# Optimization experiments

Hardware: AMD Instinct MI355X
Metric: run time of the kernel (lower is better)

Reference implementation:

```python
import jax, jax.numpy as jnp
import numpy as np

NUM_ROUTES = 1152
NUM_CAPS = 10
CAPS_IN = 8
CAPS_DIM = 16
BATCH = 128
NUM_IT = 3


def _squash(s):
    # s: [..., caps_dim]; scale = |s|^2 / ((1+|s|^2) * |s|)
    sqn = jnp.sum(s * s, axis=-1, keepdims=True)
    return s * (sqn / ((1.0 + sqn) * jnp.sqrt(sqn)))


def setup_inputs() -> dict:
    key = jax.random.key(0)
    k1, k2 = jax.random.split(key)
    x = jax.random.normal(k1, (BATCH, NUM_ROUTES, CAPS_IN), dtype=jnp.float32)
    W = jax.random.normal(k2, (1, NUM_ROUTES, NUM_CAPS, CAPS_DIM, CAPS_IN), dtype=jnp.float32)
    return {"input": x, "W": W}


def reference(input, W):
    # u_hat[b,r,j,d] = W[r,j,d,c] @ x[b,r,c]  (original broadcasts W over batch)
    u_hat = jnp.einsum('rjdc,brc->brjd', W[0], input)
    r, j = u_hat.shape[1], u_hat.shape[2]
    b_ij = jnp.zeros((r, j), dtype=u_hat.dtype)  # shared across batch, as in original
    v = None
    for _ in range(NUM_IT):
        c_ij = jax.nn.softmax(b_ij, axis=1)          # softmax over num_caps (dim=2 orig)
        s = jnp.einsum('rj,brjd->bjd', c_ij, u_hat)  # weighted sum over routes
        v = _squash(s)                                # [bs, num_caps, caps_dim]
        # agreement: <u_hat, v> averaged over batch (original updates every iter)
        b_ij = b_ij + jnp.mean(jnp.einsum('brjd,bjd->brj', u_hat, v), axis=0)
    return v[..., None]  # [bs, num_caps, caps_dim, 1], matches v_j.squeeze(1) shape
```

## Files before the change

### kernel.cpp

```cpp
#include <hip/hip_runtime.h>
#include <math.h>

#define R_ROUTES 1152
#define N_CAPS 10
#define C_IN 8
#define D_DIM 16
#define B_BATCH 128
#define JD 160
#define KK 9216
#define KSPLIT 48
#define RS 24
#define NG 5

typedef __attribute__((ext_vector_type(8))) short short8;
typedef __attribute__((ext_vector_type(4))) float f32x4;

__device__ inline unsigned short f2bf(float f) {
    unsigned int u = __float_as_uint(f);
    unsigned int r = u + 0x7FFFu + ((u >> 16) & 1u);
    return (unsigned short)(r >> 16);
}
__device__ inline float bf2f(unsigned short h) {
    return __uint_as_float(((unsigned int)h) << 16);
}


__global__ __launch_bounds__(256) void k_prep(
    const float* __restrict__ x, unsigned short* __restrict__ xh,
    unsigned short* __restrict__ xl, unsigned short* __restrict__ xT,
    float* __restrict__ b_ij, float* __restrict__ s_all) {
    __shared__ float tile[32][33];
    int bx = blockIdx.x;
    int by = blockIdx.y;
    int t = threadIdx.x;
    int tx = t & 31, ty = t >> 5;
#pragma unroll
    for (int i = 0; i < 4; i++) {
        int row = ty + i * 8;
        size_t idx = (size_t)(by * 32 + row) * KK + bx * 32 + tx;
        float v = x[idx];
        tile[row][tx] = v;
        unsigned short hi = f2bf(v);
        xh[idx] = hi;
        xl[idx] = f2bf(v - bf2f(hi));
    }
    __syncthreads();
#pragma unroll
    for (int i = 0; i < 4; i++) {
        int row = ty + i * 8;
        xT[(size_t)(bx * 32 + row) * B_BATCH + by * 32 + tx] = f2bf(tile[tx][row]);
    }
    int bid = by * 288 + bx;
    if (bid < 240) s_all[bid * 256 + t] = 0.f;
    else if (bid < 285) b_ij[(bid - 240) * 256 + t] = 0.f;
}

template <bool FIRST>
__global__ __launch_bounds__(256) void k_iter(
    const unsigned short* __restrict__ xh, const unsigned short* __restrict__ xl,
    const float* __restrict__ W, const float* __restrict__ b_ij,
    float* __restrict__ s) {
    __shared__ float cs[RS][N_CAPS];
    __shared__ unsigned short bhs[32][200];
    __shared__ unsigned short bls[32][200];
    int t = threadIdx.x;
    int ks = blockIdx.x, ng = blockIdx.y;
    int r0 = ks * RS, jd0 = ng * 32;

    if (!FIRST && t < RS) {
        float bj[N_CAPS], m = -1e30f;
#pragma unroll
        for (int j = 0; j < N_CAPS; j++) { bj[j] = b_ij[(r0 + t) * N_CAPS + j]; m = fmaxf(m, bj[j]); }
        float sum = 0.f;
#pragma unroll
        for (int j = 0; j < N_CAPS; j++) { bj[j] = expf(bj[j] - m); sum += bj[j]; }
        float inv = 1.f / sum;
#pragma unroll
        for (int j = 0; j < N_CAPS; j++) cs[t][j] = bj[j] * inv;
    }
    __syncthreads();

#pragma unroll
    for (int p = t; p < RS * 32; p += 256) {
        int rl = p >> 5, jdl = p & 31;
        const float* wp = W + ((size_t)(r0 + rl) * JD + jd0 + jdl) * C_IN;
        float c = FIRST ? 0.1f : cs[rl][(jd0 + jdl) >> 4];
        short8 vh, vl;
#pragma unroll
        for (int i = 0; i < 8; i++) {
            float cw = wp[i] * c;
            unsigned short hi = f2bf(cw);
            vh[i] = (short)hi;
            vl[i] = (short)f2bf(cw - bf2f(hi));
        }
        *(short8*)&bhs[jdl][rl * 8] = vh;
        *(short8*)&bls[jdl][rl * 8] = vl;
    }
    __syncthreads();

    int w = t >> 6, l = t & 63, row = l & 15, quad = l >> 4;
    const short8* pah0 = (const short8*)(xh + (size_t)(w * 16 + row) * KK + ks * 192);
    const short8* pal0 = (const short8*)(xl + (size_t)(w * 16 + row) * KK + ks * 192);
    const short8* pah1 = (const short8*)(xh + (size_t)((w + 4) * 16 + row) * KK + ks * 192);
    const short8* pal1 = (const short8*)(xl + (size_t)((w + 4) * 16 + row) * KK + ks * 192);
    f32x4 a00 = {0,0,0,0}, a01 = {0,0,0,0}, a10 = {0,0,0,0}, a11 = {0,0,0,0};
#pragma unroll
    for (int st = 0; st < 6; st++) {
        short8 Bh0 = *(const short8*)&bhs[row][st * 32 + quad * 8];
        short8 Bl0 = *(const short8*)&bls[row][st * 32 + quad * 8];
        short8 Bh1 = *(const short8*)&bhs[16 + row][st * 32 + quad * 8];
        short8 Bl1 = *(const short8*)&bls[16 + row][st * 32 + quad * 8];
        short8 Ah0 = pah0[st * 4 + quad], Al0 = pal0[st * 4 + quad];
        short8 Ah1 = pah1[st * 4 + quad], Al1 = pal1[st * 4 + quad];
        a00 = __builtin_amdgcn_mfma_f32_16x16x32_bf16(Ah0, Bh0, a00, 0, 0, 0);
        a00 = __builtin_amdgcn_mfma_f32_16x16x32_bf16(Ah0, Bl0, a00, 0, 0, 0);
        a00 = __builtin_amdgcn_mfma_f32_16x16x32_bf16(Al0, Bh0, a00, 0, 0, 0);
        a01 = __builtin_amdgcn_mfma_f32_16x16x32_bf16(Ah0, Bh1, a01, 0, 0, 0);
        a01 = __builtin_amdgcn_mfma_f32_16x16x32_bf16(Ah0, Bl1, a01, 0, 0, 0);
        a01 = __builtin_amdgcn_mfma_f32_16x16x32_bf16(Al0, Bh1, a01, 0, 0, 0);
        a10 = __builtin_amdgcn_mfma_f32_16x16x32_bf16(Ah1, Bh0, a10, 0, 0, 0);
        a10 = __builtin_amdgcn_mfma_f32_16x16x32_bf16(Ah1, Bl0, a10, 0, 0, 0);
        a10 = __builtin_amdgcn_mfma_f32_16x16x32_bf16(Al1, Bh0, a10, 0, 0, 0);
        a11 = __builtin_amdgcn_mfma_f32_16x16x32_bf16(Ah1, Bh1, a11, 0, 0, 0);
        a11 = __builtin_amdgcn_mfma_f32_16x16x32_bf16(Ah1, Bl1, a11, 0, 0, 0);
        a11 = __builtin_amdgcn_mfma_f32_16x16x32_bf16(Al1, Bh1, a11, 0, 0, 0);
    }
#pragma unroll
    for (int i = 0; i < 4; i++) {
        int b0 = w * 16 + quad * 4 + i, b1 = b0 + 64;
        atomicAdd(&s[(size_t)b0 * JD + jd0 + row],      a00[i]);
        atomicAdd(&s[(size_t)b0 * JD + jd0 + 16 + row], a01[i]);
        atomicAdd(&s[(size_t)b1 * JD + jd0 + row],      a10[i]);
        atomicAdd(&s[(size_t)b1 * JD + jd0 + 16 + row], a11[i]);
    }
}

__global__ __launch_bounds__(256) void k_va(
    const unsigned short* __restrict__ xT, const float* __restrict__ s,
    const float* __restrict__ W, float* __restrict__ b_ij) {
    __shared__ unsigned short vb[JD][136];
    __shared__ float m2[32][164];
    int t = threadIdx.x;
    int r0 = blockIdx.x * 4, rc0 = blockIdx.x * 32;

#pragma unroll
    for (int q = 0; q < 5; q++) {
        int pi = t * 5 + q;
        int b = pi / N_CAPS, j = pi % N_CAPS;
        const float* sp = s + (size_t)b * JD + j * D_DIM;
        float sv[D_DIM], sqn = 0.f;
#pragma unroll
        for (int d = 0; d < D_DIM; d++) { sv[d] = sp[d]; sqn = fmaf(sv[d], sv[d], sqn); }
        float scale = sqn / ((1.f + sqn) * sqrtf(sqn));
#pragma unroll
        for (int d = 0; d < D_DIM; d++)
            vb[j * D_DIM + d][b] = f2bf(sv[d] * scale);
    }
    __syncthreads();

    int w = t >> 6, l = t & 63, row = l & 15, quad = l >> 4;
    for (int u = w; u < 20; u += 4) {
        int mt = u / 10, nt = u % 10;
        const short8* pa = (const short8*)(xT + (size_t)(rc0 + mt * 16 + row) * B_BATCH);
        f32x4 acc = {0,0,0,0};
#pragma unroll
        for (int st = 0; st < 4; st++) {
            short8 Bv = *(const short8*)&vb[nt * 16 + row][st * 32 + quad * 8];
            acc = __builtin_amdgcn_mfma_f32_16x16x32_bf16(pa[st * 4 + quad], Bv, acc, 0, 0, 0);
        }
#pragma unroll
        for (int i = 0; i < 4; i++)
            m2[mt * 16 + quad * 4 + i][nt * 16 + row] = acc[i];
    }
    __syncthreads();

    for (int p = t; p < 640; p += 256) {
        int rl = p / JD, jd = p % JD;
        const float* wp = W + ((size_t)(r0 + rl) * JD + jd) * C_IN;
        float a = 0.f;
#pragma unroll
        for (int c = 0; c < C_IN; c++)
            a = fmaf(wp[c], m2[rl * 8 + c][jd], a);
#pragma unroll
        for (int off = 1; off < 16; off <<= 1) a += __shfl_xor(a, off, 16);
        if ((jd & 15) == 0)
            b_ij[(r0 + rl) * N_CAPS + (jd >> 4)] += a * (1.f / B_BATCH);
    }
}

__global__ __launch_bounds__(320) void k_rs_final(
    const float* __restrict__ s, float* __restrict__ out) {
    int t = threadIdx.x;
    int bloc = t / JD, jd = t % JD;
    int b = blockIdx.x * 2 + bloc;
    float acc = s[(size_t)b * JD + jd];
    float sq = acc * acc;
#pragma unroll
    for (int off = 1; off < 16; off <<= 1) sq += __shfl_xor(sq, off, 16);
    float scale = sq / ((1.f + sq) * sqrtf(sq));
    out[(size_t)b * JD + jd] = acc * scale;
}

extern "C" void kernel_launch(void* const* d_in, const int* in_sizes, int n_in,
                              void* d_out, int out_size, void* d_ws, size_t ws_size,
                              hipStream_t stream) {
    const float* x = (const float*)d_in[0];
    const float* W = (const float*)d_in[1];
    float* out = (float*)d_out;
    char* ws = (char*)d_ws;

    float*          b_ij = (float*)(ws + 0);
    float*          s0   = (float*)(ws + 46080);
    float*          s1   = (float*)(ws + 46080 + 81920);
    float*          s2   = (float*)(ws + 46080 + 163840);
    unsigned short* xh   = (unsigned short*)(ws + 292096);
    unsigned short* xl   = (unsigned short*)(ws + 2651392);
    unsigned short* xT   = (unsigned short*)(ws + 5010688);

    k_prep<<<dim3(288, 4), 256, 0, stream>>>(x, xh, xl, xT, b_ij, s0);

    k_iter<true><<<dim3(KSPLIT, NG), 256, 0, stream>>>(xh, xl, W, b_ij, s0);
    k_va<<<288, 256, 0, stream>>>(xT, s0, W, b_ij);

    k_iter<false><<<dim3(KSPLIT, NG), 256, 0, stream>>>(xh, xl, W, b_ij, s1);
    k_va<<<288, 256, 0, stream>>>(xT, s1, W, b_ij);

    k_iter<false><<<dim3(KSPLIT, NG), 256, 0, stream>>>(xh, xl, W, b_ij, s2);
    k_rs_final<<<64, 320, 0, stream>>>(s2, out);
}
```

Measured before the change: 113.4 us.

## Halve k-split size, drop W low-part MFMAs, fuse final squash, shrink k_va blocks

Doubles the number of k_iter blocks by halving the routes per block. It also drops the bf16 low-part correction of the c*W operand, cutting MFMAs from 3 to 2 per tile and halving that shared-memory staging. The last routing iteration now applies the final squash inside the last-finishing block via an atomic counter, replacing the separate k_rs_final launch. k_va uses smaller 128-thread blocks over twice as many blocks. Dropping the W low part lowers accuracy, and the final squash now runs in a single serial block.

```diff
diff --git a/kernel.cpp b/kernel.cpp
--- a/kernel.cpp
+++ b/kernel.cpp
@@ -8,9 +8,10 @@
 #define B_BATCH 128
 #define JD 160
 #define KK 9216
-#define KSPLIT 48
-#define RS 24
+#define KSPLIT 96
+#define RS 12
 #define NG 5
+#define GRID_I (KSPLIT * NG)
 
 typedef __attribute__((ext_vector_type(8))) short short8;
 typedef __attribute__((ext_vector_type(4))) float f32x4;
@@ -28,7 +29,8 @@
 __global__ __launch_bounds__(256) void k_prep(
     const float* __restrict__ x, unsigned short* __restrict__ xh,
     unsigned short* __restrict__ xl, unsigned short* __restrict__ xT,
-    float* __restrict__ b_ij, float* __restrict__ s_all) {
+    float* __restrict__ b_ij, float* __restrict__ s_all,
+    unsigned int* __restrict__ done) {
     __shared__ float tile[32][33];
     int bx = blockIdx.x;
     int by = blockIdx.y;
@@ -53,16 +55,18 @@
     int bid = by * 288 + bx;
     if (bid < 240) s_all[bid * 256 + t] = 0.f;
     else if (bid < 285) b_ij[(bid - 240) * 256 + t] = 0.f;
-}
-
-template <bool FIRST>
+    else if (bid == 285 && t == 0) *done = 0u;
+}
+
+template <bool FIRST, bool LAST>
 __global__ __launch_bounds__(256) void k_iter(
     const unsigned short* __restrict__ xh, const unsigned short* __restrict__ xl,
     const float* __restrict__ W, const float* __restrict__ b_ij,
-    float* __restrict__ s) {
+    float* __restrict__ s, unsigned int* __restrict__ done,
+    float* __restrict__ out) {
     __shared__ float cs[RS][N_CAPS];
-    __shared__ unsigned short bhs[32][200];
-    __shared__ unsigned short bls[32][200];
+    __shared__ unsigned short bhs[32][104];
+    __shared__ int islast;
     int t = threadIdx.x;
     int ks = blockIdx.x, ng = blockIdx.y;
     int r0 = ks * RS, jd0 = ng * 32;
@@ -85,83 +89,93 @@
         int rl = p >> 5, jdl = p & 31;
         const float* wp = W + ((size_t)(r0 + rl) * JD + jd0 + jdl) * C_IN;
         float c = FIRST ? 0.1f : cs[rl][(jd0 + jdl) >> 4];
-        short8 vh, vl;
-#pragma unroll
-        for (int i = 0; i < 8; i++) {
-            float cw = wp[i] * c;
-            unsigned short hi = f2bf(cw);
-            vh[i] = (short)hi;
-            vl[i] = (short)f2bf(cw - bf2f(hi));
-        }
+        short8 vh;
+#pragma unroll
+        for (int i = 0; i < 8; i++) vh[i] = (short)f2bf(wp[i] * c);
         *(short8*)&bhs[jdl][rl * 8] = vh;
-        *(short8*)&bls[jdl][rl * 8] = vl;
     }
     __syncthreads();
 
     int w = t >> 6, l = t & 63, row = l & 15, quad = l >> 4;
-    const short8* pah0 = (const short8*)(xh + (size_t)(w * 16 + row) * KK + ks * 192);
-    const short8* pal0 = (const short8*)(xl + (size_t)(w * 16 + row) * KK + ks * 192);
-    const short8* pah1 = (const short8*)(xh + (size_t)((w + 4) * 16 + row) * KK + ks * 192);
-    const short8* pal1 = (const short8*)(xl + (size_t)((w + 4) * 16 + row) * KK + ks * 192);
+    int mt0 = w, mt1 = w + 4;
+    const short8* pah0 = (const short8*)(xh + (size_t)(mt0 * 16 + row) * KK + ks * 96);
+    const short8* pal0 = (const short8*)(xl + (size_t)(mt0 * 16 + row) * KK + ks * 96);
+    const short8* pah1 = (const short8*)(xh + (size_t)(mt1 * 16 + row) * KK + ks * 96);
+    const short8* pal1 = (const short8*)(xl + (size_t)(mt1 * 16 + row) * KK + ks * 96);
     f32x4 a00 = {0,0,0,0}, a01 = {0,0,0,0}, a10 = {0,0,0,0}, a11 = {0,0,0,0};
 #pragma unroll
-    for (int st = 0; st < 6; st++) {
+    for (int st = 0; st < 3; st++) {
         short8 Bh0 = *(const short8*)&bhs[row][st * 32 + quad * 8];
-        short8 Bl0 = *(const short8*)&bls[row][st * 32 + quad * 8];
         short8 Bh1 = *(const short8*)&bhs[16 + row][st * 32 + quad * 8];
-        short8 Bl1 = *(const short8*)&bls[16 + row][st * 32 + quad * 8];
         short8 Ah0 = pah0[st * 4 + quad], Al0 = pal0[st * 4 + quad];
         short8 Ah1 = pah1[st * 4 + quad], Al1 = pal1[st * 4 + quad];
         a00 = __builtin_amdgcn_mfma_f32_16x16x32_bf16(Ah0, Bh0, a00, 0, 0, 0);
-        a00 = __builtin_amdgcn_mfma_f32_16x16x32_bf16(Ah0, Bl0, a00, 0, 0, 0);
         a00 = __builtin_amdgcn_mfma_f32_16x16x32_bf16(Al0, Bh0, a00, 0, 0, 0);
         a01 = __builtin_amdgcn_mfma_f32_16x16x32_bf16(Ah0, Bh1, a01, 0, 0, 0);
-        a01 = __builtin_amdgcn_mfma_f32_16x16x32_bf16(Ah0, Bl1, a01, 0, 0, 0);
         a01 = __builtin_amdgcn_mfma_f32_16x16x32_bf16(Al0, Bh1, a01, 0, 0, 0);
         a10 = __builtin_amdgcn_mfma_f32_16x16x32_bf16(Ah1, Bh0, a10, 0, 0, 0);
-        a10 = __builtin_amdgcn_mfma_f32_16x16x32_bf16(Ah1, Bl0, a10, 0, 0, 0);
         a10 = __builtin_amdgcn_mfma_f32_16x16x32_bf16(Al1, Bh0, a10, 0, 0, 0);
         a11 = __builtin_amdgcn_mfma_f32_16x16x32_bf16(Ah1, Bh1, a11, 0, 0, 0);
-        a11 = __builtin_amdgcn_mfma_f32_16x16x32_bf16(Ah1, Bl1, a11, 0, 0, 0);
         a11 = __builtin_amdgcn_mfma_f32_16x16x32_bf16(Al1, Bh1, a11, 0, 0, 0);
     }
 #pragma unroll
     for (int i = 0; i < 4; i++) {
-        int b0 = w * 16 + quad * 4 + i, b1 = b0 + 64;
+        int b0 = mt0 * 16 + quad * 4 + i, b1 = mt1 * 16 + quad * 4 + i;
         atomicAdd(&s[(size_t)b0 * JD + jd0 + row],      a00[i]);
         atomicAdd(&s[(size_t)b0 * JD + jd0 + 16 + row], a01[i]);
         atomicAdd(&s[(size_t)b1 * JD + jd0 + row],      a10[i]);
         atomicAdd(&s[(size_t)b1 * JD + jd0 + 16 + row], a11[i]);
     }
-}
-
-__global__ __launch_bounds__(256) void k_va(
+
+    if (LAST) {
+        __syncthreads();
+        if (t == 0) {
+            __threadfence();
+            unsigned int old = atomicAdd(done, 1u);
+            islast = (old == GRID_I - 1);
+        }
+        __syncthreads();
+        if (islast) {
+            __threadfence();
+#pragma unroll 4
+            for (int i = 0; i < 80; i++) {
+                int idx = i * 256 + t;
+                int b = idx / JD, jd = idx % JD;
+                float acc = s[(size_t)b * JD + jd];
+                float sq = acc * acc;
+#pragma unroll
+                for (int off = 1; off < 16; off <<= 1) sq += __shfl_xor(sq, off, 16);
+                float scale = sq / ((1.f + sq) * sqrtf(sq));
+                out[(size_t)b * JD + jd] = acc * scale;
+            }
+        }
+    }
+}
+
+__global__ __launch_bounds__(128) void k_va(
     const unsigned short* __restrict__ xT, const float* __restrict__ s,
     const float* __restrict__ W, float* __restrict__ b_ij) {
     __shared__ unsigned short vb[JD][136];
-    __shared__ float m2[32][164];
+    __shared__ float m2[16][164];
     int t = threadIdx.x;
-    int r0 = blockIdx.x * 4, rc0 = blockIdx.x * 32;
-
-#pragma unroll
-    for (int q = 0; q < 5; q++) {
-        int pi = t * 5 + q;
-        int b = pi / N_CAPS, j = pi % N_CAPS;
-        const float* sp = s + (size_t)b * JD + j * D_DIM;
+    int r0 = blockIdx.x * 2, rc0 = blockIdx.x * 16;
+
+#pragma unroll
+    for (int q = 0; q < N_CAPS; q++) {
+        const float* sp = s + (size_t)t * JD + q * D_DIM;
         float sv[D_DIM], sqn = 0.f;
 #pragma unroll
         for (int d = 0; d < D_DIM; d++) { sv[d] = sp[d]; sqn = fmaf(sv[d], sv[d], sqn); }
         float scale = sqn / ((1.f + sqn) * sqrtf(sqn));
 #pragma unroll
         for (int d = 0; d < D_DIM; d++)
-            vb[j * D_DIM + d][b] = f2bf(sv[d] * scale);
+            vb[q * D_DIM + d][t] = f2bf(sv[d] * scale);
     }
     __syncthreads();
 
     int w = t >> 6, l = t & 63, row = l & 15, quad = l >> 4;
-    for (int u = w; u < 20; u += 4) {
-        int mt = u / 10, nt = u % 10;
-        const short8* pa = (const short8*)(xT + (size_t)(rc0 + mt * 16 + row) * B_BATCH);
+    const short8* pa = (const short8*)(xT + (size_t)(rc0 + row) * B_BATCH);
+    for (int nt = w; nt < N_CAPS; nt += 2) {
         f32x4 acc = {0,0,0,0};
 #pragma unroll
         for (int st = 0; st < 4; st++) {
@@ -170,11 +184,11 @@
         }
 #pragma unroll
         for (int i = 0; i < 4; i++)
-            m2[mt * 16 + quad * 4 + i][nt * 16 + row] = acc[i];
-    }
-    __syncthreads();
-
-    for (int p = t; p < 640; p += 256) {
+            m2[quad * 4 + i][nt * 16 + row] = acc[i];
+    }
+    __syncthreads();
+
+    for (int p = t; p < 2 * JD; p += 128) {
         int rl = p / JD, jd = p % JD;
         const float* wp = W + ((size_t)(r0 + rl) * JD + jd) * C_IN;
         float a = 0.f;
@@ -186,19 +200,6 @@
         if ((jd & 15) == 0)
             b_ij[(r0 + rl) * N_CAPS + (jd >> 4)] += a * (1.f / B_BATCH);
     }
-}
-
-__global__ __launch_bounds__(320) void k_rs_final(
-    const float* __restrict__ s, float* __restrict__ out) {
-    int t = threadIdx.x;
-    int bloc = t / JD, jd = t % JD;
-    int b = blockIdx.x * 2 + bloc;
-    float acc = s[(size_t)b * JD + jd];
-    float sq = acc * acc;
-#pragma unroll
-    for (int off = 1; off < 16; off <<= 1) sq += __shfl_xor(sq, off, 16);
-    float scale = sq / ((1.f + sq) * sqrtf(sq));
-    out[(size_t)b * JD + jd] = acc * scale;
 }
 
 extern "C" void kernel_launch(void* const* d_in, const int* in_sizes, int n_in,
@@ -213,18 +214,18 @@
     float*          s0   = (float*)(ws + 46080);
     float*          s1   = (float*)(ws + 46080 + 81920);
     float*          s2   = (float*)(ws + 46080 + 163840);
+    unsigned int*   done = (unsigned int*)(ws + 291840);
     unsigned short* xh   = (unsigned short*)(ws + 292096);
     unsigned short* xl   = (unsigned short*)(ws + 2651392);
     unsigned short* xT   = (unsigned short*)(ws + 5010688);
 
-    k_prep<<<dim3(288, 4), 256, 0, stream>>>(x, xh, xl, xT, b_ij, s0);
-
-    k_iter<true><<<dim3(KSPLIT, NG), 256, 0, stream>>>(xh, xl, W, b_ij, s0);
-    k_va<<<288, 256, 0, stream>>>(xT, s0, W, b_ij);
-
-    k_iter<false><<<dim3(KSPLIT, NG), 256, 0, stream>>>(xh, xl, W, b_ij, s1);
-    k_va<<<288, 256, 0, stream>>>(xT, s1, W, b_ij);
-
-    k_iter<false><<<dim3(KSPLIT, NG), 256, 0, stream>>>(xh, xl, W, b_ij, s2);
-    k_rs_final<<<64, 320, 0, stream>>>(s2, out);
-}
+    k_prep<<<dim3(288, 4), 256, 0, stream>>>(x, xh, xl, xT, b_ij, s0, done);
+
+    k_iter<true, false><<<dim3(KSPLIT, NG), 256, 0, stream>>>(xh, xl, W, b_ij, s0, done, out);
+    k_va<<<576, 128, 0, stream>>>(xT, s0, W, b_ij);
+
+    k_iter<false, false><<<dim3(KSPLIT, NG), 256, 0, stream>>>(xh, xl, W, b_ij, s1, done, out);
+    k_va<<<576, 128, 0, stream>>>(xT, s1, W, b_ij);
+
+    k_iter<false, true><<<dim3(KSPLIT, NG), 256, 0, stream>>>(xh, xl, W, b_ij, s2, done, out);
+}
```

New measurement: 152.3 us. 1.34x slower.
